# Performance work log

Measured on AMD Instinct MI355X. Metric: run time of the kernel, lower is better.

The kernel has to match this reference:

```python
import jax, jax.numpy as jnp
import numpy as np

VOCAB = 32000
HID = 1024
CUTOFFS = [0, 10000, 20000, 32000]
N_CLUSTERS = 2
DIV = 4
PROJ_DIMS = [HID // DIV**i for i in range(N_CLUSTERS + 1)]  # [1024, 256, 64]
# Faithful to source quirk: n_vocabs = cutoffs[i] + cutoffs[i+1]
LOGIT_DIMS = [CUTOFFS[i] + CUTOFFS[i + 1] for i in range(N_CLUSTERS + 1)]  # [10000, 30000, 52000]


def setup_inputs() -> dict:
    key = jax.random.key(0)
    ks = jax.random.split(key, 16)
    N = 2048
    inp = {
        "x": jax.random.normal(ks[0], (N, HID), dtype=jnp.float32),
        "y": jax.random.randint(ks[1], (N,), 0, VOCAB, dtype=jnp.int64),
    }
    s = 0.02
    # projections: Linear(hidden, proj_dims[i], bias=False); stored as [in, out]
    inp["Wp0"] = jax.random.normal(ks[2], (HID, PROJ_DIMS[0]), dtype=jnp.float32) * s
    inp["Wp1"] = jax.random.normal(ks[3], (HID, PROJ_DIMS[1]), dtype=jnp.float32) * s
    inp["Wp2"] = jax.random.normal(ks[4], (HID, PROJ_DIMS[2]), dtype=jnp.float32) * s
    # logits: Linear(proj_dims[i], LOGIT_DIMS[i]) with bias
    inp["Wl0"] = jax.random.normal(ks[5], (PROJ_DIMS[0], LOGIT_DIMS[0]), dtype=jnp.float32) * s
    inp["bl0"] = jnp.zeros((LOGIT_DIMS[0],), dtype=jnp.float32)
    inp["Wl1"] = jax.random.normal(ks[6], (PROJ_DIMS[1], LOGIT_DIMS[1]), dtype=jnp.float32) * s
    inp["bl1"] = jnp.zeros((LOGIT_DIMS[1],), dtype=jnp.float32)
    inp["Wl2"] = jax.random.normal(ks[7], (PROJ_DIMS[2], LOGIT_DIMS[2]), dtype=jnp.float32) * s
    inp["bl2"] = jnp.zeros((LOGIT_DIMS[2],), dtype=jnp.float32)
    # cluster_logit: Linear(hidden, n_clusters)
    inp["Wc"] = jax.random.normal(ks[8], (HID, N_CLUSTERS), dtype=jnp.float32) * s
    inp["bc"] = jnp.zeros((N_CLUSTERS,), dtype=jnp.float32)
    return inp


def reference(x, y, Wp0, Wp1, Wp2, Wl0, bl0, Wl1, bl1, Wl2, bl2, Wc, bc):
    # head: project (dim-preserving here) then head-vocab logits + cluster logits
    head_proj = x @ Wp0                                   # [N, 1024]
    head_logit = jnp.concatenate(
        [head_proj @ Wl0 + bl0, head_proj @ Wc + bc], axis=1
    )                                                     # [N, 10000 + 2]
    head_lp = jax.nn.log_softmax(head_logit, axis=1)

    nll = jnp.zeros(y.shape, dtype=x.dtype)

    # cluster 0: targets in [0, cutoffs[1])
    m0 = (y >= CUTOFFS[0]) & (y < CUTOFFS[1])
    t0 = jnp.clip(y - CUTOFFS[0], 0, head_lp.shape[1] - 1)
    lp0 = jnp.take_along_axis(head_lp, t0[:, None], axis=1)[:, 0]
    nll = jnp.where(m0, -lp0, nll)

    # tail clusters: small projection GEMM + log_softmax + gather, combined via masks
    tails = [(Wp1, Wl1, bl1), (Wp2, Wl2, bl2)]
    for i, (Wp, Wl, bl) in enumerate(tails, start=1):
        l, r = CUTOFFS[i], CUTOFFS[i + 1]
        mask = (y >= l) & (y < r)
        t = jnp.clip(y - l, 0, Wl.shape[1] - 1)
        tail_lp = jax.nn.log_softmax((x @ Wp) @ Wl + bl, axis=1)  # [N, LOGIT_DIMS[i]]
        # faithful to source: head column -i (reversed cluster order quirk)
        lp = head_lp[:, -i] + jnp.take_along_axis(tail_lp, t[:, None], axis=1)[:, 0]
        nll = jnp.where(mask, -lp, nll)

    return nll
```

## Files before the change

kernel.cpp:

```cpp
#include <hip/hip_runtime.h>
#include <math.h>

#define HID 1024
#define NROWS 2048

typedef __attribute__((ext_vector_type(8))) short short8;
typedef __attribute__((ext_vector_type(4))) short short4_t;
typedef __attribute__((ext_vector_type(4))) float f32x4;

__device__ __forceinline__ short f2bf(float f) {
  union { float f; unsigned u; } v; v.f = f;
  unsigned r = v.u + 0x7fffu + ((v.u >> 16) & 1u);
  return (short)(r >> 16);
}
__device__ __forceinline__ float bf2f(short s) {
  union { unsigned u; float f; } v; v.u = ((unsigned)(unsigned short)s) << 16;
  return v.f;
}
__device__ __forceinline__ float wave_sum(float a) {
#pragma unroll
  for (int off = 32; off; off >>= 1) a += __shfl_xor(a, off, 64);
  return a;
}

__global__ __launch_bounds__(256) void prep(
    const float* __restrict__ x, const int* __restrict__ y,
    const float* __restrict__ Wp0, const float* __restrict__ Wp1,
    const float* __restrict__ Wp2, const float* __restrict__ Wl0,
    const float* __restrict__ Wl1, const float* __restrict__ Wl2,
    short* __restrict__ xb,
    int* __restrict__ counts, int* __restrict__ slot_of_row,
    int* __restrict__ rows1, int* __restrict__ rows2,
    short* __restrict__ T0, short* __restrict__ T1, short* __restrict__ T2,
    short* __restrict__ T3, short* __restrict__ T4, short* __restrict__ T5) {
  const int tid = threadIdx.x;
  int b = blockIdx.x;
  if (b == 0) {
    __shared__ int c1s, c2s;
    if (tid == 0) { c1s = 0; c2s = 0; }
    __syncthreads();
    for (int r = tid; r < NROWS; r += 256) {
      const int yy = y[r];
      if (yy >= 20000) {
        const int s = atomicAdd(&c2s, 1);
        slot_of_row[r] = s; rows2[s] = r;
      } else if (yy >= 10000) {
        const int s = atomicAdd(&c1s, 1);
        slot_of_row[r] = s; rows1[s] = r;
      } else {
        slot_of_row[r] = -1;
      }
    }
    __syncthreads();
    if (tid == 0) { counts[0] = NROWS; counts[1] = c1s; counts[2] = c2s; }
    return;
  }
  if (b <= 512) {
    const int base = (b - 1) * 4096;
#pragma unroll
    for (int j = 0; j < 4; ++j) {
      const int i = base + j * 1024 + tid * 4;
      const float4 v = *(const float4*)&x[i];
      short4_t o;
      o.x = f2bf(v.x); o.y = f2bf(v.y); o.z = f2bf(v.z); o.w = f2bf(v.w);
      *(short4_t*)&xb[i] = o;
    }
    return;
  }
  b -= 513;
  const float* W; short* BT; int K, N, Npad, tn;
  if (b < 256)               { W = Wp0; BT = T0; K = 1024; N = 1024;  Npad = 1024;  tn = 16;  }
  else if ((b -= 256) < 64)  { W = Wp1; BT = T1; K = 1024; N = 256;   Npad = 256;   tn = 4;   }
  else if ((b -= 64) < 32)   { W = Wp2; BT = T2; K = 1024; N = 64;    Npad = 128;   tn = 2;   }
  else if ((b -= 32) < 2560) { W = Wl0; BT = T3; K = 1024; N = 10000; Npad = 10240; tn = 160; }
  else if ((b -= 2560) < 1888){W = Wl1; BT = T4; K = 256;  N = 30000; Npad = 30208; tn = 472; }
  else { b -= 1888;            W = Wl2; BT = T5; K = 64;   N = 52000; Npad = 52224; tn = 816; }

  __shared__ float T[64][65];
  const int n0 = (b % tn) * 64, k0 = (b / tn) * 64;
  const int rr = tid >> 4, cc = (tid & 15) * 4;
#pragma unroll
  for (int j = 0; j < 4; ++j) {
    const int kr = rr + j * 16;
    const float* p = &W[(size_t)(k0 + kr) * N + n0 + cc];
    float v0 = 0.f, v1 = 0.f, v2 = 0.f, v3 = 0.f;
    if (n0 + cc + 3 < N) {
      const float4 v = *(const float4*)p;
      v0 = v.x; v1 = v.y; v2 = v.z; v3 = v.w;
    } else {
      if (n0 + cc + 0 < N) v0 = p[0];
      if (n0 + cc + 1 < N) v1 = p[1];
      if (n0 + cc + 2 < N) v2 = p[2];
    }
    T[kr][cc] = v0; T[kr][cc + 1] = v1; T[kr][cc + 2] = v2; T[kr][cc + 3] = v3;
  }
  __syncthreads();
  const int nl = tid >> 2, ks = (tid & 3) * 16;
  const int n = n0 + nl;
  if (n < Npad) {
    const bool z = (n >= N);
    short* dst = &BT[(size_t)n * K + k0 + ks];
#pragma unroll
    for (int h = 0; h < 2; ++h) {
      short8 o;
#pragma unroll
      for (int e = 0; e < 8; ++e)
        o[e] = z ? (short)0 : f2bf(T[ks + h * 8 + e][nl]);
      *(short8*)(dst + h * 8) = o;
    }
  }
}

#define GLOAD_LDS(g, l)                                                      \
  __builtin_amdgcn_global_load_lds(                                          \
      (const __attribute__((address_space(1))) void*)(g),                    \
      (__attribute__((address_space(3))) void*)(l), 16, 0, 0)

#define BARR do { asm volatile("" ::: "memory");                             \
                  __builtin_amdgcn_s_barrier();                              \
                  asm volatile("" ::: "memory"); } while (0)

#define VMW(n) asm volatile("s_waitcnt vmcnt(" #n ")" ::: "memory")

#define LGKM0 do { asm volatile("s_waitcnt lgkmcnt(0)" ::: "memory");        \
                   __builtin_amdgcn_sched_barrier(0); } while (0)

__device__ __forceinline__ void stage_half(const short* __restrict__ src,
                                           size_t row0, int kOff, short* dst,
                                           int stride, int w, int rsub, int kc) {
  const short* g0 = src + (row0 + (size_t)(w * 8 + rsub)) * (size_t)stride
                    + kOff + kc * 8;
  GLOAD_LDS(g0, dst + w * 512);
  GLOAD_LDS(g0 + (size_t)64 * stride, dst + 4096 + w * 512);
}

#define RD_A8(dst, base) do {                                                \
  _Pragma("unroll") for (int mt = 0; mt < 4; ++mt)                           \
  _Pragma("unroll") for (int kk = 0; kk < 2; ++kk)                           \
    dst[mt * 2 + kk] = *(const short8*)((base) +                             \
        (pm * 64 + mt * 16 + ln) * 64 + (((kk * 4 + quad) ^ l7) << 3));      \
} while (0)

#define RD_B4(dst, base) do {                                                \
  _Pragma("unroll") for (int nt = 0; nt < 2; ++nt)                           \
  _Pragma("unroll") for (int kk = 0; kk < 2; ++kk)                           \
    dst[nt * 2 + kk] = *(const short8*)((base) +                             \
        (pn * 32 + nt * 16 + ln) * 64 + (((kk * 4 + quad) ^ l7) << 3));      \
} while (0)

#define MFMA16(ACC, ar, br) do {                                             \
  __builtin_amdgcn_s_setprio(1);                                             \
  _Pragma("unroll") for (int mt = 0; mt < 4; ++mt)                           \
  _Pragma("unroll") for (int nt = 0; nt < 2; ++nt)                           \
  _Pragma("unroll") for (int kk = 0; kk < 2; ++kk)                           \
    ACC[mt][nt] = __builtin_amdgcn_mfma_f32_16x16x32_bf16(                   \
        ar[mt * 2 + kk], br[nt * 2 + kk], ACC[mt][nt], 0, 0, 0);             \
  __builtin_amdgcn_s_setprio(0);                                             \
} while (0)

__device__ __forceinline__ void gemm256_8ph(
    const short* __restrict__ A, const short* __restrict__ BT,
    int K, int NT, size_t rowA0, size_t rowB0, short* lds,
    f32x4 acc[2][2][4][2], int w, int lane) {
  const int quad = lane >> 4, ln = lane & 15, l7 = lane & 7;
  const int pm = w >> 2, pn = w & 3;
  const int rsub = lane >> 3, kc = (lane & 7) ^ rsub;
  short* const Ab0 = lds;
  short* const Ab1 = lds + 16384;
  short* const Bb0 = lds + 32768;
  short* const Bb1 = lds + 49152;

  if (NT == 1) {
    stage_half(A,  rowA0,       0, Ab0,        K, w, rsub, kc);
    stage_half(BT, rowB0,       0, Bb0,        K, w, rsub, kc);
    stage_half(BT, rowB0 + 128, 0, Bb0 + 8192, K, w, rsub, kc);
    stage_half(A,  rowA0 + 128, 0, Ab0 + 8192, K, w, rsub, kc);
    VMW(0);
    BARR;
    short8 aq0[8], aq1[8], bq0[4], bq1[4];
    RD_A8(aq0, Ab0); RD_B4(bq0, Bb0);
    BARR; LGKM0; MFMA16(acc[0][0], aq0, bq0); BARR;
    RD_B4(bq1, Bb0 + 8192);
    BARR; LGKM0; MFMA16(acc[0][1], aq0, bq1); BARR;
    RD_A8(aq1, Ab0 + 8192);
    BARR; LGKM0; MFMA16(acc[1][1], aq1, bq1); BARR;
    MFMA16(acc[1][0], aq1, bq0);
    return;
  }

  stage_half(A,  rowA0,       0,  Ab0,        K, w, rsub, kc);
  stage_half(BT, rowB0,       0,  Bb0,        K, w, rsub, kc);
  stage_half(BT, rowB0 + 128, 0,  Bb0 + 8192, K, w, rsub, kc);
  stage_half(A,  rowA0 + 128, 0,  Ab0 + 8192, K, w, rsub, kc);
  stage_half(A,  rowA0,       64, Ab1,        K, w, rsub, kc);
  stage_half(BT, rowB0,       64, Bb1,        K, w, rsub, kc);
  stage_half(BT, rowB0 + 128, 64, Bb1 + 8192, K, w, rsub, kc);
  stage_half(A,  rowA0 + 128, 64, Ab1 + 8192, K, w, rsub, kc);
  VMW(8);
  BARR;

  const int NI = NT >> 1;
  for (int i = 0; i < NI; ++i) {
    const int t0 = 2 * i;
    const bool more = (t0 + 2 < NT);
    const int ku0 = (t0 + 2) << 6, ku1 = (t0 + 3) << 6;
    short8 aq0[8], aq1[8], bq0[4], bq1[4];
    RD_A8(aq0, Ab0); RD_B4(bq0, Bb0);
    BARR; LGKM0; MFMA16(acc[0][0], aq0, bq0); BARR;
    RD_B4(bq1, Bb0 + 8192);
    if (more) stage_half(A, rowA0, ku0, Ab0, K, w, rsub, kc);
    BARR; LGKM0; MFMA16(acc[0][1], aq0, bq1); BARR;
    RD_A8(aq1, Ab0 + 8192);
    if (more) stage_half(BT, rowB0, ku0, Bb0, K, w, rsub, kc);
    BARR; LGKM0; MFMA16(acc[1][1], aq1, bq1); BARR;
    if (more) {
      stage_half(BT, rowB0 + 128, ku0, Bb0 + 8192, K, w, rsub, kc);
      stage_half(A,  rowA0 + 128, ku0, Ab0 + 8192, K, w, rsub, kc);
      VMW(8);
    } else {
      VMW(0);
    }
    BARR; MFMA16(acc[1][0], aq1, bq0); BARR;
    RD_A8(aq0, Ab1); RD_B4(bq0, Bb1);
    BARR; LGKM0; MFMA16(acc[0][0], aq0, bq0); BARR;
    RD_B4(bq1, Bb1 + 8192);
    if (more) stage_half(A, rowA0, ku1, Ab1, K, w, rsub, kc);
    BARR; LGKM0; MFMA16(acc[0][1], aq0, bq1); BARR;
    RD_A8(aq1, Ab1 + 8192);
    if (more) stage_half(BT, rowB0, ku1, Bb1, K, w, rsub, kc);
    BARR; LGKM0; MFMA16(acc[1][1], aq1, bq1); BARR;
    if (more) {
      stage_half(BT, rowB0 + 128, ku1, Bb1 + 8192, K, w, rsub, kc);
      stage_half(A,  rowA0 + 128, ku1, Ab1 + 8192, K, w, rsub, kc);
      VMW(8);
    }
    BARR; MFMA16(acc[1][0], aq1, bq0); BARR;
  }
}


__device__ __forceinline__ void exp_epilogue(
    f32x4 acc[2][2][4][2], const float* __restrict__ bias,
    float* __restrict__ ps, size_t c0, int Ncols, int nsplit, int r0,
    short* lds, int tid, int w, int lane) {
  const int quad = lane >> 4, ln = lane & 15;
  const int pm = w >> 2, pn = w & 3;
  float bv[2][2];
#pragma unroll
  for (int qb = 0; qb < 2; ++qb)
#pragma unroll
    for (int nt = 0; nt < 2; ++nt) {
      const size_t cg = c0 + qb * 128 + pn * 32 + nt * 16 + ln;
      bv[qb][nt] = (cg < (size_t)Ncols) ? bias[cg] : -1.0e30f;
    }
  float* const psF = (float*)lds;
  BARR;
#pragma unroll
  for (int qa = 0; qa < 2; ++qa)
#pragma unroll
    for (int qb = 0; qb < 2; ++qb)
#pragma unroll
      for (int mt = 0; mt < 4; ++mt)
#pragma unroll
        for (int r = 0; r < 4; ++r) {
          float s = __expf(acc[qa][qb][mt][0][r] + bv[qb][0]) +
                    __expf(acc[qa][qb][mt][1][r] + bv[qb][1]);
#pragma unroll
          for (int off = 1; off < 16; off <<= 1) s += __shfl_xor(s, off, 64);
          if (ln == 0)
            psF[(pn * 2 + qb) * 256 + qa * 128 + pm * 64 + mt * 16 + quad * 4 + r] = s;
        }
  BARR;
  {
    const int qb = tid >> 8, row = tid & 255;
    const int cs = (int)(c0 >> 7) + qb;
    if (cs < nsplit)
      ps[(size_t)(r0 + row) * nsplit + cs] =
          psF[(0 * 2 + qb) * 256 + row] + psF[(1 * 2 + qb) * 256 + row] +
          psF[(2 * 2 + qb) * 256 + row] + psF[(3 * 2 + qb) * 256 + row];
  }
}

__device__ __forceinline__ void mfma_mainloop(const short* aB[4], const short* bB[4],
                                              short* As, short* Bs,
                                              f32x4 acc[4][4],
                                              int K, int w, int lane) {
  const int quad = lane >> 4, ln = lane & 15;
  const int wm = w >> 1, wn = w & 1;
  const int l7 = ln & 7;
  for (int kt = 0; kt < K; kt += 64) {
#pragma unroll
    for (int i = 0; i < 4; ++i) {
      const int row = w * 32 + i * 8;
      __builtin_amdgcn_global_load_lds(
          (const __attribute__((address_space(1))) void*)(aB[i] + kt),
          (__attribute__((address_space(3))) void*)(As + row * 64), 16, 0, 0);
      __builtin_amdgcn_global_load_lds(
          (const __attribute__((address_space(1))) void*)(bB[i] + kt),
          (__attribute__((address_space(3))) void*)(Bs + row * 64), 16, 0, 0);
    }
    __syncthreads();
#pragma unroll
    for (int ks = 0; ks < 2; ++ks) {
      const int kcs = ks * 4 + quad;
      short8 af[4], bfr[4];
#pragma unroll
      for (int mt = 0; mt < 4; ++mt) {
        const int row = wm * 64 + mt * 16 + ln;
        af[mt] = *(const short8*)(As + ((row * 8 + (kcs ^ l7)) << 3));
      }
#pragma unroll
      for (int nt = 0; nt < 4; ++nt) {
        const int rowb = wn * 64 + nt * 16 + ln;
        bfr[nt] = *(const short8*)(Bs + ((rowb * 8 + (kcs ^ l7)) << 3));
      }
#pragma unroll
      for (int mt = 0; mt < 4; ++mt)
#pragma unroll
        for (int nt = 0; nt < 4; ++nt)
          acc[mt][nt] = __builtin_amdgcn_mfma_f32_16x16x32_bf16(
              af[mt], bfr[nt], acc[mt][nt], 0, 0, 0);
    }
    __syncthreads();
  }
}

__global__ __launch_bounds__(256) void proj_all(
    const short* __restrict__ xb,
    const short* __restrict__ WpT0, const short* __restrict__ WpT1,
    const short* __restrict__ WpT2,
    short* __restrict__ P0b, short* __restrict__ P1c, short* __restrict__ P2c,
    const int* __restrict__ rows1, const int* __restrict__ rows2,
    const int* __restrict__ counts) {
  int b = blockIdx.x;
  const short* BT; short* C; int N, r0, c0, cnt;
  const int* rowlist = nullptr;
  if (b < 128) {
    BT = WpT0; C = P0b; N = 1024;
    c0 = (b & 7) * 128; r0 = (b >> 3) * 128; cnt = NROWS;
  } else if (b < 160) {
    b -= 128; BT = WpT1; C = P1c; N = 256;
    c0 = (b & 1) * 128; r0 = (b >> 1) * 128; rowlist = rows1; cnt = counts[1];
  } else {
    b -= 160; BT = WpT2; C = P2c; N = 64;
    c0 = 0; r0 = b * 128; rowlist = rows2; cnt = counts[2];
  }
  if (r0 >= cnt) return;

  __shared__ short As[128 * 64];
  __shared__ short Bs[128 * 64];
  const int tid = threadIdx.x;
  const int w = tid >> 6, lane = tid & 63;
  const int quad = lane >> 4, ln = lane & 15;
  const int wm = w >> 1, wn = w & 1;
  const int rsub = lane >> 3;
  const int kc = (lane & 7) ^ rsub;
  const int K = 1024;

  const short* aB[4]; const short* bB[4];
#pragma unroll
  for (int i = 0; i < 4; ++i) {
    const int sl = r0 + w * 32 + i * 8 + rsub;
    const int ar = rowlist ? rowlist[sl < cnt ? sl : cnt - 1] : sl;
    aB[i] = xb + (size_t)ar * K + kc * 8;
    bB[i] = BT + (size_t)(c0 + w * 32 + i * 8 + rsub) * K + kc * 8;
  }

  f32x4 acc[4][4];
  const f32x4 zero = {0.f, 0.f, 0.f, 0.f};
#pragma unroll
  for (int i = 0; i < 4; ++i)
#pragma unroll
    for (int j = 0; j < 4; ++j) acc[i][j] = zero;
  mfma_mainloop(aB, bB, As, Bs, acc, K, w, lane);
#pragma unroll
  for (int mt = 0; mt < 4; ++mt)
#pragma unroll
    for (int r = 0; r < 4; ++r) {
      const int grow = r0 + wm * 64 + mt * 16 + quad * 4 + r;
#pragma unroll
      for (int nt = 0; nt < 4; ++nt) {
        const int cg = c0 + wn * 64 + nt * 16 + ln;
        if (cg < N) C[(size_t)grow * N + cg] = f2bf(acc[mt][nt][r]);
      }
    }
}

__global__ __launch_bounds__(512, 2) void logit_fused(
    const short* __restrict__ P0b, const short* __restrict__ WlT0,
    const float* __restrict__ bl0, float* __restrict__ psh,
    const short* __restrict__ P1c, const short* __restrict__ WlT1,
    const float* __restrict__ bl1, float* __restrict__ ps1,
    const short* __restrict__ P2c, const short* __restrict__ WlT2,
    const float* __restrict__ bl2, float* __restrict__ ps2,
    const int* __restrict__ counts) {
  __shared__ short lds[65536];
  const int tid = threadIdx.x;
  const int w = tid >> 6, lane = tid & 63;
  const int b = blockIdx.x;

  const short* A; const short* BT; const float* bias; float* ps;
  int K, NT, Ncols, nsplit, r0; size_t c0;
  if (b < 320) {
    const int xcd = b & 7, j = b >> 3;
    const int cb = xcd * 5 + j % 5, rb = j / 5;
    r0 = rb * 256; c0 = (size_t)cb * 256;
    A = P0b; BT = WlT0; bias = bl0; ps = psh;
    K = 1024; NT = 16; Ncols = 10000; nsplit = 79;
  } else if (b < 1264) {
    const int b1 = b - 320;
    const int rb = b1 / 118, cb = b1 % 118;
    r0 = rb * 256;
    if (r0 >= counts[1]) return;
    c0 = (size_t)cb * 256;
    A = P1c; BT = WlT1; bias = bl1; ps = ps1;
    K = 256; NT = 4; Ncols = 30000; nsplit = 235;
  } else {
    const int b2 = b - 1264;
    const int rb = b2 / 204, cb = b2 % 204;
    r0 = rb * 256;
    if (r0 >= counts[2]) return;
    c0 = (size_t)cb * 256;
    A = P2c; BT = WlT2; bias = bl2; ps = ps2;
    K = 64; NT = 1; Ncols = 52000; nsplit = 407;
  }

  f32x4 acc[2][2][4][2];
  const f32x4 zero = {0.f, 0.f, 0.f, 0.f};
#pragma unroll
  for (int qa = 0; qa < 2; ++qa)
#pragma unroll
    for (int qb = 0; qb < 2; ++qb)
#pragma unroll
      for (int mt = 0; mt < 4; ++mt)
#pragma unroll
        for (int nt = 0; nt < 2; ++nt) acc[qa][qb][mt][nt] = zero;

  gemm256_8ph(A, BT, K, NT, (size_t)r0, c0, lds, acc, w, lane);
  exp_epilogue(acc, bias, ps, c0, Ncols, nsplit, r0, lds, tid, w, lane);
}

__global__ __launch_bounds__(256) void finalize(
    const short* __restrict__ P0b, const short* __restrict__ P1c,
    const short* __restrict__ P2c,
    const short* __restrict__ WlT0, const float* __restrict__ bl0,
    const short* __restrict__ WlT1, const float* __restrict__ bl1,
    const short* __restrict__ WlT2, const float* __restrict__ bl2,
    const float* __restrict__ Wc, const float* __restrict__ bc,
    const int* __restrict__ y, const int* __restrict__ slot_of_row,
    const float* __restrict__ psh, const float* __restrict__ ps1,
    const float* __restrict__ ps2, float* __restrict__ out) {
  const int lane = threadIdx.x & 63;
  const int row = blockIdx.x * 4 + (threadIdx.x >> 6);

  float a0 = 0.f, a1 = 0.f;
  for (int k = lane; k < HID; k += 64) {
    const float p = bf2f(P0b[(size_t)row * HID + k]);
    a0 += p * Wc[2 * k];
    a1 += p * Wc[2 * k + 1];
  }
  a0 = wave_sum(a0);
  a1 = wave_sum(a1);
  const float cl0 = a0 + bc[0], cl1 = a1 + bc[1];

  float S = 0.f;
  for (int i = lane; i < 79; i += 64) S += psh[(size_t)row * 79 + i];
  S = wave_sum(S) + __expf(cl0) + __expf(cl1);
  const float lse = logf(S);

  const int yy = y[row];
  float nll;
  if (yy < 10000) {
    const short* pr = P0b + (size_t)row * 1024;
    const short* wr = WlT0 + (size_t)yy * 1024;
    float a = 0.f;
    for (int kk = lane * 4; kk < 1024; kk += 256) {
      const short4_t p = *(const short4_t*)(pr + kk);
      const short4_t wv = *(const short4_t*)(wr + kk);
      a += bf2f(p.x) * bf2f(wv.x) + bf2f(p.y) * bf2f(wv.y)
         + bf2f(p.z) * bf2f(wv.z) + bf2f(p.w) * bf2f(wv.w);
    }
    a = wave_sum(a);
    nll = -((a + bl0[yy]) - lse);
  } else if (yy < 20000) {
    const int t = yy - 10000;
    const int slot = slot_of_row[row];
    float S1 = 0.f;
    for (int i = lane; i < 235; i += 64) S1 += ps1[(size_t)slot * 235 + i];
    S1 = wave_sum(S1);
    const short* pr = P1c + (size_t)slot * 256;
    const short* wr = WlT1 + (size_t)t * 256;
    const int kk = lane * 4;
    const short4_t p = *(const short4_t*)(pr + kk);
    const short4_t wv = *(const short4_t*)(wr + kk);
    float a = bf2f(p.x) * bf2f(wv.x) + bf2f(p.y) * bf2f(wv.y)
            + bf2f(p.z) * bf2f(wv.z) + bf2f(p.w) * bf2f(wv.w);
    a = wave_sum(a);
    nll = -((cl1 - lse) + ((a + bl1[t]) - logf(S1)));
  } else {
    const int t = yy - 20000;
    const int slot = slot_of_row[row];
    float S2 = 0.f;
    for (int i = lane; i < 407; i += 64) S2 += ps2[(size_t)slot * 407 + i];
    S2 = wave_sum(S2);
    float a = 0.f;
    if (lane < 16) {
      const short* pr = P2c + (size_t)slot * 64;
      const short* wr = WlT2 + (size_t)t * 64;
      const int kk = lane * 4;
      const short4_t p = *(const short4_t*)(pr + kk);
      const short4_t wv = *(const short4_t*)(wr + kk);
      a = bf2f(p.x) * bf2f(wv.x) + bf2f(p.y) * bf2f(wv.y)
        + bf2f(p.z) * bf2f(wv.z) + bf2f(p.w) * bf2f(wv.w);
    }
    a = wave_sum(a);
    nll = -((cl0 - lse) + ((a + bl2[t]) - logf(S2)));
  }
  if (lane == 0) out[row] = nll;
}

extern "C" void kernel_launch(void* const* d_in, const int* in_sizes, int n_in,
                              void* d_out, int out_size, void* d_ws, size_t ws_size,
                              hipStream_t stream) {
  const float* x   = (const float*)d_in[0];
  const int*   y   = (const int*)d_in[1];
  const float* Wp0 = (const float*)d_in[2];
  const float* Wp1 = (const float*)d_in[3];
  const float* Wp2 = (const float*)d_in[4];
  const float* Wl0 = (const float*)d_in[5];
  const float* bl0 = (const float*)d_in[6];
  const float* Wl1 = (const float*)d_in[7];
  const float* bl1 = (const float*)d_in[8];
  const float* Wl2 = (const float*)d_in[9];
  const float* bl2 = (const float*)d_in[10];
  const float* Wc  = (const float*)d_in[11];
  const float* bc  = (const float*)d_in[12];
  float* out = (float*)d_out;

  float* fws = (float*)d_ws;
  float* psh = fws; fws += (size_t)NROWS * 79;
  float* ps1 = fws; fws += (size_t)NROWS * 235;
  float* ps2 = fws; fws += (size_t)NROWS * 407;
  int* iws = (int*)fws;
  int* counts      = iws; iws += 4;
  int* slot_of_row = iws; iws += NROWS;
  int* rows1       = iws; iws += NROWS;
  int* rows2       = iws; iws += NROWS;
  short* sp = (short*)iws;
  short* xb   = sp; sp += (size_t)NROWS * 1024;
  short* P0b  = sp; sp += (size_t)NROWS * 1024;
  short* P1c  = sp; sp += (size_t)NROWS * 256;
  short* P2c  = sp; sp += (size_t)NROWS * 64;
  short* WpT0 = sp; sp += (size_t)1024 * 1024;
  short* WpT1 = sp; sp += (size_t)256 * 1024;
  short* WpT2 = sp; sp += (size_t)128 * 1024;
  short* WlT0 = sp; sp += (size_t)10240 * 1024;
  short* WlT1 = sp; sp += (size_t)30208 * 256;
  short* WlT2 = sp; sp += (size_t)52224 * 64;

  dim3 blk(256);
  prep<<<dim3(6129), blk, 0, stream>>>(x, y, Wp0, Wp1, Wp2, Wl0, Wl1, Wl2,
                                       xb, counts, slot_of_row, rows1, rows2,
                                       WpT0, WpT1, WpT2, WlT0, WlT1, WlT2);
  proj_all<<<dim3(176), blk, 0, stream>>>(xb, WpT0, WpT1, WpT2, P0b, P1c, P2c,
                                          rows1, rows2, counts);
  logit_fused<<<dim3(2896), dim3(512), 0, stream>>>(
      P0b, WlT0, bl0, psh, P1c, WlT1, bl1, ps1, P2c, WlT2, bl2, ps2, counts);
  finalize<<<dim3(NROWS / 4), blk, 0, stream>>>(
      P0b, P1c, P2c, WlT0, bl0, WlT1, bl1, WlT2, bl2, Wc, bc, y, slot_of_row,
      psh, ps1, ps2, out);
}
```

Measured before the change: 322.3 us.

## Software-pipeline LDS fragment reads ahead of MFMAs with partial lgkmcnt waits

Restructures the 256x256 GEMM main loop so the LDS register reads for the next MFMA phase are issued before the current phase's MFMAs. It waits on partial lgkmcnt/vmcnt counts instead of draining to zero, and halves the number of barriers per phase. The NT==1 path now issues all LDS reads up front with a single wait. This aims to hide LDS latency and reduce barrier stalls, at the cost of extra fragment registers (separate b0E/b0O buffers) and fragile hand-counted wait values that could cause races if they are wrong.

```diff
diff --git a/kernel.cpp b/kernel.cpp
--- a/kernel.cpp
+++ b/kernel.cpp
@@ -122,8 +122,8 @@
 
 #define VMW(n) asm volatile("s_waitcnt vmcnt(" #n ")" ::: "memory")
 
-#define LGKM0 do { asm volatile("s_waitcnt lgkmcnt(0)" ::: "memory");        \
-                   __builtin_amdgcn_sched_barrier(0); } while (0)
+#define LGKMC(n) do { asm volatile("s_waitcnt lgkmcnt(" #n ")" ::: "memory"); \
+                      __builtin_amdgcn_sched_barrier(0); } while (0)
 
 __device__ __forceinline__ void stage_half(const short* __restrict__ src,
                                            size_t row0, int kOff, short* dst,
@@ -158,7 +158,7 @@
   __builtin_amdgcn_s_setprio(0);                                             \
 } while (0)
 
-__device__ __forceinline__ void gemm256_8ph(
+__device__ __forceinline__ void gemm256_pipe(
     const short* __restrict__ A, const short* __restrict__ BT,
     int K, int NT, size_t rowA0, size_t rowB0, short* lds,
     f32x4 acc[2][2][4][2], int w, int lane) {
@@ -170,6 +170,8 @@
   short* const Bb0 = lds + 32768;
   short* const Bb1 = lds + 49152;
 
+  short8 a0[8], a1[8], b1[4], b0E[4], b0O[4];
+
   if (NT == 1) {
     stage_half(A,  rowA0,       0, Ab0,        K, w, rsub, kc);
     stage_half(BT, rowB0,       0, Bb0,        K, w, rsub, kc);
@@ -177,14 +179,13 @@
     stage_half(A,  rowA0 + 128, 0, Ab0 + 8192, K, w, rsub, kc);
     VMW(0);
     BARR;
-    short8 aq0[8], aq1[8], bq0[4], bq1[4];
-    RD_A8(aq0, Ab0); RD_B4(bq0, Bb0);
-    BARR; LGKM0; MFMA16(acc[0][0], aq0, bq0); BARR;
-    RD_B4(bq1, Bb0 + 8192);
-    BARR; LGKM0; MFMA16(acc[0][1], aq0, bq1); BARR;
-    RD_A8(aq1, Ab0 + 8192);
-    BARR; LGKM0; MFMA16(acc[1][1], aq1, bq1); BARR;
-    MFMA16(acc[1][0], aq1, bq0);
+    RD_A8(a0, Ab0); RD_B4(b0E, Bb0);
+    RD_B4(b1, Bb0 + 8192); RD_A8(a1, Ab0 + 8192);
+    LGKMC(0);
+    MFMA16(acc[0][0], a0, b0E);
+    MFMA16(acc[0][1], a0, b1);
+    MFMA16(acc[1][1], a1, b1);
+    MFMA16(acc[1][0], a1, b0E);
     return;
   }
 
@@ -194,47 +195,74 @@
   stage_half(A,  rowA0 + 128, 0,  Ab0 + 8192, K, w, rsub, kc);
   stage_half(A,  rowA0,       64, Ab1,        K, w, rsub, kc);
   stage_half(BT, rowB0,       64, Bb1,        K, w, rsub, kc);
+  VMW(4);
+  BARR;
+  RD_A8(a0, Ab0);
+  RD_B4(b0E, Bb0);
   stage_half(BT, rowB0 + 128, 64, Bb1 + 8192, K, w, rsub, kc);
   stage_half(A,  rowA0 + 128, 64, Ab1 + 8192, K, w, rsub, kc);
-  VMW(8);
-  BARR;
 
   const int NI = NT >> 1;
   for (int i = 0; i < NI; ++i) {
     const int t0 = 2 * i;
     const bool more = (t0 + 2 < NT);
     const int ku0 = (t0 + 2) << 6, ku1 = (t0 + 3) << 6;
-    short8 aq0[8], aq1[8], bq0[4], bq1[4];
-    RD_A8(aq0, Ab0); RD_B4(bq0, Bb0);
-    BARR; LGKM0; MFMA16(acc[0][0], aq0, bq0); BARR;
-    RD_B4(bq1, Bb0 + 8192);
+    RD_B4(b1, Bb0 + 8192);
+    LGKMC(4);
+    MFMA16(acc[0][0], a0, b0E);
+    BARR;
+    RD_A8(a1, Ab0 + 8192);
     if (more) stage_half(A, rowA0, ku0, Ab0, K, w, rsub, kc);
-    BARR; LGKM0; MFMA16(acc[0][1], aq0, bq1); BARR;
-    RD_A8(aq1, Ab0 + 8192);
+    LGKMC(8);
+    MFMA16(acc[0][1], a0, b1);
+    if (more) { VMW(8); } else { VMW(6); }
+    BARR;
+    RD_A8(a0, Ab1);
     if (more) stage_half(BT, rowB0, ku0, Bb0, K, w, rsub, kc);
-    BARR; LGKM0; MFMA16(acc[1][1], aq1, bq1); BARR;
+    LGKMC(8);
+    MFMA16(acc[1][1], a1, b1);
+    if (more) { VMW(8); } else { VMW(4); }
+    BARR;
+    RD_B4(b0O, Bb1);
     if (more) {
       stage_half(BT, rowB0 + 128, ku0, Bb0 + 8192, K, w, rsub, kc);
       stage_half(A,  rowA0 + 128, ku0, Ab0 + 8192, K, w, rsub, kc);
-      VMW(8);
+    }
+    LGKMC(4);
+    MFMA16(acc[1][0], a1, b0E);
+    if (more) { VMW(8); } else { VMW(0); }
+    BARR;
+    RD_B4(b1, Bb1 + 8192);
+    LGKMC(4);
+    MFMA16(acc[0][0], a0, b0O);
+    BARR;
+    RD_A8(a1, Ab1 + 8192);
+    if (more) stage_half(A, rowA0, ku1, Ab1, K, w, rsub, kc);
+    LGKMC(8);
+    MFMA16(acc[0][1], a0, b1);
+    if (more) { VMW(8); }
+    BARR;
+    if (more) {
+      RD_A8(a0, Ab0);
+      stage_half(BT, rowB0, ku1, Bb1, K, w, rsub, kc);
+      LGKMC(8);
     } else {
-      VMW(0);
-    }
-    BARR; MFMA16(acc[1][0], aq1, bq0); BARR;
-    RD_A8(aq0, Ab1); RD_B4(bq0, Bb1);
-    BARR; LGKM0; MFMA16(acc[0][0], aq0, bq0); BARR;
-    RD_B4(bq1, Bb1 + 8192);
-    if (more) stage_half(A, rowA0, ku1, Ab1, K, w, rsub, kc);
-    BARR; LGKM0; MFMA16(acc[0][1], aq0, bq1); BARR;
-    RD_A8(aq1, Ab1 + 8192);
-    if (more) stage_half(BT, rowB0, ku1, Bb1, K, w, rsub, kc);
-    BARR; LGKM0; MFMA16(acc[1][1], aq1, bq1); BARR;
+      LGKMC(0);
+    }
+    MFMA16(acc[1][1], a1, b1);
+    if (more) { VMW(8); }
+    BARR;
     if (more) {
+      RD_B4(b0E, Bb0);
       stage_half(BT, rowB0 + 128, ku1, Bb1 + 8192, K, w, rsub, kc);
       stage_half(A,  rowA0 + 128, ku1, Ab1 + 8192, K, w, rsub, kc);
-      VMW(8);
-    }
-    BARR; MFMA16(acc[1][0], aq1, bq0); BARR;
+      LGKMC(4);
+    } else {
+      LGKMC(0);
+    }
+    MFMA16(acc[1][0], a1, b0O);
+    if (more) { VMW(8); }
+    BARR;
   }
 }
 
@@ -436,7 +464,7 @@
 #pragma unroll
         for (int nt = 0; nt < 2; ++nt) acc[qa][qb][mt][nt] = zero;
 
-  gemm256_8ph(A, BT, K, NT, (size_t)r0, c0, lds, acc, w, lane);
+  gemm256_pipe(A, BT, K, NT, (size_t)r0, c0, lds, acc, w, lane);
   exp_epilogue(acc, bias, ps, c0, Ncols, nsplit, r0, lds, tid, w, lane);
 }
 
```

Measured after the change: 402.1 us. 24.8% more time.
